# Performance work log

Measured on AMD Instinct MI355X. Metric: run time of the kernel, lower is better.

Reference implementation:

```python
import jax, jax.numpy as jnp
import numpy as np

B, L, D = 1, 2048, 768
H, DH = 12, 64  # n_heads, d_head (D // H)
LN_EPS = 1e-5
DEN_EPS = 1e-6


def setup_inputs() -> dict:
    key = jax.random.key(0)
    ks = jax.random.split(key, 11)
    s = 0.02
    return {
        "x": jax.random.normal(ks[0], (B, L, D), dtype=jnp.float32),
        "W_qkv": jax.random.normal(ks[1], (D, 3 * D), dtype=jnp.float32) * s,
        "b_qkv": jnp.zeros((3 * D,), dtype=jnp.float32),
        "W_sem": jax.random.normal(ks[2], (D, 2 * D), dtype=jnp.float32) * s,
        "b_sem": jnp.zeros((2 * D,), dtype=jnp.float32),
        "W_ctx": jax.random.normal(ks[3], (D, 2 * D), dtype=jnp.float32) * s,
        "b_ctx": jnp.zeros((2 * D,), dtype=jnp.float32),
        "W_proj": jax.random.normal(ks[4], (D, D), dtype=jnp.float32) * s,
        "b_proj": jnp.zeros((D,), dtype=jnp.float32),
        "ln_g": jnp.ones((D,), dtype=jnp.float32),
        "ln_b": jnp.zeros((D,), dtype=jnp.float32),
    }


def _heads(t):
    # [B,L,D] -> [B,H,L,DH]
    return t.reshape(B, L, H, DH).transpose(0, 2, 1, 3)


def reference(x, W_qkv, b_qkv, W_sem, b_sem, W_ctx, b_ctx, W_proj, b_proj, ln_g, ln_b):
    # LayerNorm
    mu = jnp.mean(x, axis=-1, keepdims=True)
    var = jnp.mean(jnp.square(x - mu), axis=-1, keepdims=True)
    x_norm = (x - mu) * jax.lax.rsqrt(var + LN_EPS) * ln_g + ln_b

    qkv = x_norm @ W_qkv + b_qkv
    q, k, v = jnp.split(qkv, 3, axis=-1)

    # interference gate from raw x
    sem = x @ W_sem + b_sem
    sem_amp = jax.nn.softplus(sem[..., :D])
    sem_phase = sem[..., D:]
    ctx = x @ W_ctx + b_ctx
    ctx_amp = jax.nn.softplus(ctx[..., :D])
    ctx_phase = ctx[..., D:]
    gate = jax.nn.sigmoid(sem_amp * ctx_amp * jnp.cos(sem_phase - ctx_phase))
    k = k * gate

    q_f = jax.nn.elu(_heads(q)) + 1.0  # [B,H,L,DH]
    k_f = jax.nn.elu(_heads(k)) + 1.0
    v_f = _heads(v)

    # causal linear attention: cumsum of kv outer products along L
    kv = jnp.einsum("bhld,bhle->bhlde", k_f, v_f)  # [B,H,L,DH,DH]
    kv_cum = jnp.cumsum(kv, axis=2)
    out_num = jnp.einsum("bhld,bhlde->bhle", q_f, kv_cum)  # [B,H,L,DH]

    k_cum = jnp.cumsum(k_f, axis=2)
    out_den = jnp.sum(q_f * k_cum, axis=-1, keepdims=True) + DEN_EPS

    attn = (out_num / out_den).transpose(0, 2, 1, 3).reshape(B, L, D)
    return attn @ W_proj + b_proj
```

## Files before the change

kernel.cpp:

```cpp
#include <hip/hip_runtime.h>
#include <math.h>

#define LSEQ 2048
#define DMODEL 768
#define NHEAD 12
#define DHEAD 64
#define NCHUNK 32
#define NMERGED 5376

typedef unsigned short ushort_t;
typedef __attribute__((ext_vector_type(8))) short short8;
typedef float float4v __attribute__((ext_vector_type(4)));

__device__ __forceinline__ ushort_t f2b(float f) {
    union { float f; unsigned int u; } v; v.f = f;
    unsigned int u = v.u;
    return (ushort_t)((u + 0x7fffu + ((u >> 16) & 1u)) >> 16);
}
__device__ __forceinline__ float b2f(ushort_t u) {
    union { unsigned int u; float f; } v; v.u = ((unsigned int)u) << 16;
    return v.f;
}

__device__ __forceinline__ void gl_lds16(const ushort_t* g, ushort_t* l) {
    __builtin_amdgcn_global_load_lds(
        (const __attribute__((address_space(1))) unsigned int*)g,
        (__attribute__((address_space(3))) unsigned int*)l, 16, 0, 0);
}

__global__ void pre_kernel(const float* __restrict__ x, const float* __restrict__ g,
                           const float* __restrict__ beta, ushort_t* __restrict__ xn,
                           ushort_t* __restrict__ xb,
                           const float* __restrict__ Wq, const float* __restrict__ Ws,
                           const float* __restrict__ Wc, ushort_t* __restrict__ Tm,
                           const float* __restrict__ Wp, ushort_t* __restrict__ Tp) {
    __shared__ float red[4];
    __shared__ float bc;
    __shared__ float tile[32][33];
    int tid = threadIdx.x;
    if (blockIdx.x < 2048) {
        int row = blockIdx.x;
        const float* xr = x + (size_t)row * DMODEL;
        float v0 = xr[tid], v1 = xr[tid + 256], v2 = xr[tid + 512];
        float s = v0 + v1 + v2;
#pragma unroll
        for (int o = 32; o > 0; o >>= 1) s += __shfl_down(s, o);
        if ((tid & 63) == 0) red[tid >> 6] = s;
        __syncthreads();
        if (tid == 0) bc = (red[0] + red[1] + red[2] + red[3]) * (1.0f / DMODEL);
        __syncthreads();
        float mu = bc;
        float d0 = v0 - mu, d1 = v1 - mu, d2 = v2 - mu;
        float vs = d0 * d0 + d1 * d1 + d2 * d2;
        __syncthreads();
#pragma unroll
        for (int o = 32; o > 0; o >>= 1) vs += __shfl_down(vs, o);
        if ((tid & 63) == 0) red[tid >> 6] = vs;
        __syncthreads();
        if (tid == 0) bc = rsqrtf((red[0] + red[1] + red[2] + red[3]) * (1.0f / DMODEL) + 1e-5f);
        __syncthreads();
        float r = bc;
        ushort_t* xo = xn + (size_t)row * DMODEL;
        ushort_t* xc = xb + (size_t)row * DMODEL;
        xo[tid]       = f2b(d0 * r * g[tid]       + beta[tid]);
        xo[tid + 256] = f2b(d1 * r * g[tid + 256] + beta[tid + 256]);
        xo[tid + 512] = f2b(d2 * r * g[tid + 512] + beta[tid + 512]);
        xc[tid]       = f2b(v0);
        xc[tid + 256] = f2b(v1);
        xc[tid + 512] = f2b(v2);
    } else {
        int bid = blockIdx.x - 2048;
        int nb = bid % 72;
        int kb = (bid / 72) % 24;
        int zb = bid / (72 * 24);
        const float* W; ushort_t* Wt; int N;
        switch (zb) {
            case 0: W = Wq; Wt = Tm;                        N = 2304; break;
            case 1: W = Ws; Wt = Tm + (size_t)2304 * 768;   N = 1536; break;
            case 2: W = Wc; Wt = Tm + (size_t)3840 * 768;   N = 1536; break;
            default: W = Wp; Wt = Tp;                       N = 768;  break;
        }
        int nbase = nb * 32;
        if (nbase >= N) return;
        int tr = tid >> 5, tc = tid & 31;
        int kbase = kb * 32;
#pragma unroll
        for (int p = 0; p < 4; p++) {
            int r = p * 8 + tr;
            tile[r][tc] = W[(size_t)(kbase + r) * N + nbase + tc];
        }
        __syncthreads();
#pragma unroll
        for (int p = 0; p < 4; p++) {
            int r = p * 8 + tr;
            Wt[(size_t)(nbase + r) * 768 + kbase + tc] = f2b(tile[tc][r]);
        }
    }
}

__global__ __launch_bounds__(256) void gemm_merged_kernel(
    const ushort_t* __restrict__ Axn, const ushort_t* __restrict__ Axb,
    const ushort_t* __restrict__ Bt,
    const float* __restrict__ b_qkv, const float* __restrict__ b_sem,
    const float* __restrict__ b_ctx, ushort_t* __restrict__ Cb,
    ushort_t* __restrict__ vb) {
    const int K = 768;
    __shared__ ushort_t As[128 * 32];
    __shared__ ushort_t Bs[128 * 32];
    __shared__ ushort_t Ct[128 * 132];
    int tid = threadIdx.x;
    int wave = tid >> 6, lane = tid & 63;
    int wm = (wave >> 1) * 64, wn = (wave & 1) * 64;
    int quad = lane >> 4, l16 = lane & 15;
    int bid = blockIdx.x;
    int xcd = bid & 7, slot = bid >> 3;
    int tile_id = xcd * 84 + slot;
    int m0 = (tile_id & 15) * 128;
    int n0 = (tile_id >> 4) * 128;
    const ushort_t* A = (n0 < 2304) ? Axn : Axb;
    const float* bias = (n0 < 2304) ? (b_qkv + n0) : (n0 < 3840 ? (b_sem + n0 - 2304) : (b_ctx + n0 - 3840));

    int r0 = tid >> 2;
    int kc = ((tid & 3) ^ ((r0 >> 1) & 3)) * 8;
    const ushort_t* Ag0 = A + (size_t)(m0 + r0) * K + kc;
    const ushort_t* Ag1 = A + (size_t)(m0 + 64 + r0) * K + kc;
    const ushort_t* Bg0 = Bt + (size_t)(n0 + r0) * K + kc;
    const ushort_t* Bg1 = Bt + (size_t)(n0 + 64 + r0) * K + kc;
    ushort_t* Al0 = &As[(wave * 64) * 8];
    ushort_t* Al1 = &As[(256 + wave * 64) * 8];
    ushort_t* Bl0 = &Bs[(wave * 64) * 8];
    ushort_t* Bl1 = &Bs[(256 + wave * 64) * 8];

    float4v acc[4][4];
#pragma unroll
    for (int i = 0; i < 4; i++)
#pragma unroll
        for (int j = 0; j < 4; j++)
#pragma unroll
            for (int r = 0; r < 4; r++) acc[i][j][r] = 0.0f;

    for (int k0 = 0; k0 < K; k0 += 32) {
        gl_lds16(Ag0 + k0, Al0);
        gl_lds16(Ag1 + k0, Al1);
        gl_lds16(Bg0 + k0, Bl0);
        gl_lds16(Bg1 + k0, Bl1);
        __syncthreads();
        short8 af[4], bf[4];
#pragma unroll
        for (int i = 0; i < 4; i++) {
            int rr = wm + i * 16 + l16;
            af[i] = *(const short8*)&As[rr * 32 + ((quad ^ ((rr >> 1) & 3)) * 8)];
        }
#pragma unroll
        for (int j = 0; j < 4; j++) {
            int rr = wn + j * 16 + l16;
            bf[j] = *(const short8*)&Bs[rr * 32 + ((quad ^ ((rr >> 1) & 3)) * 8)];
        }
#pragma unroll
        for (int i = 0; i < 4; i++)
#pragma unroll
            for (int j = 0; j < 4; j++)
                acc[i][j] = __builtin_amdgcn_mfma_f32_16x16x32_bf16(af[i], bf[j], acc[i][j], 0, 0, 0);
        __syncthreads();
    }
#pragma unroll
    for (int i = 0; i < 4; i++) {
#pragma unroll
        for (int j = 0; j < 4; j++) {
            int colb = wn + j * 16 + l16;
            float bv = bias[colb];
#pragma unroll
            for (int r = 0; r < 4; r++) {
                int row = wm + i * 16 + quad * 4 + r;
                Ct[row * 132 + colb] = f2b(acc[i][j][r] + bv);
            }
        }
    }
    __syncthreads();
    bool is_v = (n0 >= 1536 && n0 < 2304);
    int rr0 = tid >> 4;
    int cc0 = (tid & 15) * 8;
#pragma unroll
    for (int p = 0; p < 8; p++) {
        int r = p * 16 + rr0;
        uint4 vdat = *(const uint4*)&Ct[r * 132 + cc0];
        int grow = m0 + r;
        if (is_v) {
            *(uint4*)&vb[(size_t)grow * DMODEL + (n0 - 1536) + cc0] = vdat;
        } else {
            *(uint4*)&Cb[(size_t)grow * NMERGED + n0 + cc0] = vdat;
        }
    }
}

__global__ __launch_bounds__(256) void gemm_64_kernel(
    const ushort_t* __restrict__ A, const ushort_t* __restrict__ Bt,
    const float* __restrict__ bias, float* __restrict__ C,
    int N, int K) {
    __shared__ ushort_t As[64 * 32];
    __shared__ ushort_t Bs[64 * 32];
    int tid = threadIdx.x;
    int wave = tid >> 6, lane = tid & 63;
    int wm = (wave >> 1) * 32, wn = (wave & 1) * 32;
    int quad = lane >> 4, l16 = lane & 15;
    int m0 = blockIdx.y * 64, n0 = blockIdx.x * 64;

    int r0 = tid >> 2;
    int kc = ((tid & 3) ^ ((r0 >> 1) & 3)) * 8;
    const ushort_t* Ag = A + (size_t)(m0 + r0) * K + kc;
    const ushort_t* Bg = Bt + (size_t)(n0 + r0) * K + kc;
    ushort_t* Al = &As[(wave * 16) * 32];
    ushort_t* Bl = &Bs[(wave * 16) * 32];

    float4v acc[2][2];
#pragma unroll
    for (int i = 0; i < 2; i++)
#pragma unroll
        for (int j = 0; j < 2; j++)
#pragma unroll
            for (int r = 0; r < 4; r++) acc[i][j][r] = 0.0f;

    for (int k0 = 0; k0 < K; k0 += 32) {
        gl_lds16(Ag + k0, Al);
        gl_lds16(Bg + k0, Bl);
        __syncthreads();
        short8 af[2], bf[2];
#pragma unroll
        for (int i = 0; i < 2; i++) {
            int rr = wm + i * 16 + l16;
            af[i] = *(const short8*)&As[rr * 32 + ((quad ^ ((rr >> 1) & 3)) * 8)];
        }
#pragma unroll
        for (int j = 0; j < 2; j++) {
            int rr = wn + j * 16 + l16;
            bf[j] = *(const short8*)&Bs[rr * 32 + ((quad ^ ((rr >> 1) & 3)) * 8)];
        }
#pragma unroll
        for (int i = 0; i < 2; i++)
#pragma unroll
            for (int j = 0; j < 2; j++)
                acc[i][j] = __builtin_amdgcn_mfma_f32_16x16x32_bf16(af[i], bf[j], acc[i][j], 0, 0, 0);
        __syncthreads();
    }
#pragma unroll
    for (int i = 0; i < 2; i++) {
#pragma unroll
        for (int j = 0; j < 2; j++) {
            int col = n0 + wn + j * 16 + l16;
            float bv = bias[col];
#pragma unroll
            for (int r = 0; r < 4; r++) {
                int row = m0 + wm + i * 16 + quad * 4 + r;
                C[(size_t)row * N + col] = acc[i][j][r] + bv;
            }
        }
    }
}

__device__ __forceinline__ float softplus_f(float x) {
    return (x > 15.f) ? x : log1pf(expf(x));
}

__global__ void gate_feat_kernel(const ushort_t* __restrict__ qscb,
                                 ushort_t* __restrict__ qf, ushort_t* __restrict__ kf) {
    int t = blockIdx.x * 256 + threadIdx.x;
    int l = t / 192, d = (t - l * 192) * 4;
    size_t base = (size_t)l * NMERGED;
    ushort_t sa[4], sp[4], ca[4], cp[4], q[4], k[4];
    *(uint2*)sa = *(const uint2*)&qscb[base + 2304 + d];
    *(uint2*)sp = *(const uint2*)&qscb[base + 3072 + d];
    *(uint2*)ca = *(const uint2*)&qscb[base + 3840 + d];
    *(uint2*)cp = *(const uint2*)&qscb[base + 4608 + d];
    *(uint2*)q  = *(const uint2*)&qscb[base + d];
    *(uint2*)k  = *(const uint2*)&qscb[base + 768 + d];
    ushort_t qo[4], ko[4];
#pragma unroll
    for (int j = 0; j < 4; j++) {
        float amp = softplus_f(b2f(sa[j])) * softplus_f(b2f(ca[j]));
        float tt = amp * cosf(b2f(sp[j]) - b2f(cp[j]));
        float gate = 1.0f / (1.0f + expf(-tt));
        float kv = b2f(k[j]) * gate;
        float qv = b2f(q[j]);
        qo[j] = f2b((qv > 0.f) ? qv + 1.0f : expf(qv));
        ko[j] = f2b((kv > 0.f) ? kv + 1.0f : expf(kv));
    }
    size_t o = (size_t)l * DMODEL + d;
    *(uint2*)&qf[o] = *(uint2*)qo;
    *(uint2*)&kf[o] = *(uint2*)ko;
}

__global__ __launch_bounds__(256) void chunk_sum_mfma(const ushort_t* __restrict__ kf,
                                                      const ushort_t* __restrict__ vb,
                                                      float* __restrict__ S) {
    int h = blockIdx.x % NHEAD;
    int c = blockIdx.x / NHEAD;
    __shared__ ushort_t Kt[64 * 72];
    __shared__ ushort_t Vt[64 * 72];
    int tid = threadIdx.x;
    const size_t hb = (size_t)h * DHEAD;
#pragma unroll
    for (int it = 0; it < 4; it++) {
        int r = it * 16 + (tid >> 4);
        int cc = (tid & 15) * 4;
        int lg = c * 64 + r;
        ushort_t kt4[4], vt4[4];
        *(uint2*)kt4 = *(const uint2*)&kf[(size_t)lg * DMODEL + hb + cc];
        *(uint2*)vt4 = *(const uint2*)&vb[(size_t)lg * DMODEL + hb + cc];
#pragma unroll
        for (int i2 = 0; i2 < 4; i2++) {
            Kt[(cc + i2) * 72 + r] = kt4[i2];
            Vt[(cc + i2) * 72 + r] = vt4[i2];
        }
    }
    __syncthreads();
    int wave = tid >> 6, lane = tid & 63, quad = lane >> 4, l16 = lane & 15;
    int wm = wave * 16;
    float4v acc[4];
#pragma unroll
    for (int jt = 0; jt < 4; jt++)
#pragma unroll
        for (int r = 0; r < 4; r++) acc[jt][r] = 0.0f;
#pragma unroll
    for (int ks = 0; ks < 2; ks++) {
        short8 af = *(const short8*)&Kt[(wm + l16) * 72 + ks * 32 + quad * 8];
#pragma unroll
        for (int jt = 0; jt < 4; jt++) {
            short8 bf = *(const short8*)&Vt[(jt * 16 + l16) * 72 + ks * 32 + quad * 8];
            acc[jt] = __builtin_amdgcn_mfma_f32_16x16x32_bf16(af, bf, acc[jt], 0, 0, 0);
        }
    }
    float* Sp = S + (size_t)(h * NCHUNK + c) * 4160;
#pragma unroll
    for (int jt = 0; jt < 4; jt++) {
        float4 o;
        o.x = acc[jt][0]; o.y = acc[jt][1]; o.z = acc[jt][2]; o.w = acc[jt][3];
        *(float4*)&Sp[(jt * 16 + l16) * 64 + wm + quad * 4] = o;
    }
    if (tid < 64) {
        float s = 0.f;
#pragma unroll
        for (int g = 0; g < 8; g++) {
            short8 kv8 = *(const short8*)&Kt[tid * 72 + g * 8];
#pragma unroll
            for (int i2 = 0; i2 < 8; i2++) s += b2f(((ushort_t*)&kv8)[i2]);
        }
        Sp[4096 + tid] = s;
    }
}

__global__ void prefix_kernel(const float* __restrict__ S, ushort_t* __restrict__ Pb,
                              float* __restrict__ kpf) {
    int h = blockIdx.x;
    int i = blockIdx.y * 256 + threadIdx.x;
    if (i >= 4160) return;
    float v[NCHUNK];
    size_t base = (size_t)h * NCHUNK * 4160 + i;
#pragma unroll
    for (int c2 = 0; c2 < NCHUNK; c2++) v[c2] = S[base + (size_t)c2 * 4160];
    float run = 0.f;
    if (i < 4096) {
        size_t pb = (size_t)h * NCHUNK * 4096 + i;
#pragma unroll
        for (int c2 = 0; c2 < NCHUNK; c2++) {
            Pb[pb + (size_t)c2 * 4096] = f2b(run);
            run += v[c2];
        }
    } else {
        size_t kb = (size_t)h * NCHUNK * 64 + (i - 4096);
#pragma unroll
        for (int c2 = 0; c2 < NCHUNK; c2++) {
            kpf[kb + (size_t)c2 * 64] = run;
            run += v[c2];
        }
    }
}

__global__ __launch_bounds__(256) void attn_out_mfma(const ushort_t* __restrict__ qf,
                                                     const ushort_t* __restrict__ kf,
                                                     const ushort_t* __restrict__ vb,
                                                     const ushort_t* __restrict__ Pb,
                                                     const float* __restrict__ kpf,
                                                     ushort_t* __restrict__ attn) {
    int h = blockIdx.x % NHEAD;
    int c = blockIdx.x / NHEAD;
    __shared__ ushort_t Qs[64 * 72];
    __shared__ ushort_t Ks[64 * 72];
    __shared__ ushort_t Pt[64 * 72];
    __shared__ ushort_t Vt[64 * 72];
    __shared__ float Sc[64 * 68];
    __shared__ float kpl[64];
    __shared__ float denp[4][64];
    __shared__ float dnl[64];
    int tid = threadIdx.x;
    const size_t hb = (size_t)h * DHEAD;
    const size_t pcb = (size_t)(h * NCHUNK + c);
#pragma unroll
    for (int it = 0; it < 2; it++) {
        int chunk = it * 256 + tid;
        int r = chunk >> 3, c8 = (chunk & 7) * 8;
        int lg = c * 64 + r;
        *(uint4*)&Qs[r * 72 + c8] = *(const uint4*)&qf[(size_t)lg * DMODEL + hb + c8];
        *(uint4*)&Ks[r * 72 + c8] = *(const uint4*)&kf[(size_t)lg * DMODEL + hb + c8];
        *(uint4*)&Pt[r * 72 + c8] = *(const uint4*)&Pb[pcb * 4096 + r * 64 + c8];
    }
#pragma unroll
    for (int it = 0; it < 4; it++) {
        int r = it * 16 + (tid >> 4);
        int cc = (tid & 15) * 4;
        int lg = c * 64 + r;
        ushort_t vt4[4];
        *(uint2*)vt4 = *(const uint2*)&vb[(size_t)lg * DMODEL + hb + cc];
#pragma unroll
        for (int i2 = 0; i2 < 4; i2++) Vt[(cc + i2) * 72 + r] = vt4[i2];
    }
    if (tid < 64) kpl[tid] = kpf[pcb * 64 + tid];
    __syncthreads();
    int wave = tid >> 6, lane = tid & 63, quad = lane >> 4, l16 = lane & 15;
    int wm = wave * 16;
    float4v s_acc[4], n_acc[4];
#pragma unroll
    for (int jt = 0; jt < 4; jt++)
#pragma unroll
        for (int r = 0; r < 4; r++) { s_acc[jt][r] = 0.0f; n_acc[jt][r] = 0.0f; }
#pragma unroll
    for (int ks = 0; ks < 2; ks++) {
        short8 aq = *(const short8*)&Qs[(wm + l16) * 72 + ks * 32 + quad * 8];
#pragma unroll
        for (int jt = 0; jt < 4; jt++) {
            short8 bk = *(const short8*)&Ks[(jt * 16 + l16) * 72 + ks * 32 + quad * 8];
            short8 bp = *(const short8*)&Pt[(jt * 16 + l16) * 72 + ks * 32 + quad * 8];
            s_acc[jt] = __builtin_amdgcn_mfma_f32_16x16x32_bf16(aq, bk, s_acc[jt], 0, 0, 0);
            n_acc[jt] = __builtin_amdgcn_mfma_f32_16x16x32_bf16(aq, bp, n_acc[jt], 0, 0, 0);
        }
    }
#pragma unroll
    for (int jt = 0; jt < 4; jt++)
#pragma unroll
        for (int r = 0; r < 4; r++)
            Sc[(wm + quad * 4 + r) * 68 + jt * 16 + l16] = s_acc[jt][r];
    __syncthreads();
    {
        int l = tid & 63, part = tid >> 6;
        float s = 0.f;
#pragma unroll
        for (int jj = 0; jj < 16; jj++) {
            int j = part * 16 + jj;
            float v = Sc[l * 68 + j];
            s += (j <= l) ? v : 0.f;
        }
#pragma unroll
        for (int dd = 0; dd < 16; dd++) {
            int d = part * 16 + dd;
            s += b2f(Qs[l * 72 + d]) * kpl[d];
        }
        denp[part][l] = s;
    }
    __syncthreads();
    if (tid < 64) dnl[tid] = denp[0][tid] + denp[1][tid] + denp[2][tid] + denp[3][tid] + 1e-6f;
    __syncthreads();
#pragma unroll
    for (int ks = 0; ks < 2; ks++) {
        int m = wm + l16;
        float sv[8];
        *(float4*)&sv[0] = *(const float4*)&Sc[m * 68 + ks * 32 + quad * 8];
        *(float4*)&sv[4] = *(const float4*)&Sc[m * 68 + ks * 32 + quad * 8 + 4];
        ushort_t am[8];
#pragma unroll
        for (int i2 = 0; i2 < 8; i2++) {
            int j = ks * 32 + quad * 8 + i2;
            am[i2] = (j <= m) ? f2b(sv[i2]) : (ushort_t)0;
        }
        short8 af = *(short8*)am;
#pragma unroll
        for (int jt = 0; jt < 4; jt++) {
            short8 bv = *(const short8*)&Vt[(jt * 16 + l16) * 72 + ks * 32 + quad * 8];
            n_acc[jt] = __builtin_amdgcn_mfma_f32_16x16x32_bf16(af, bv, n_acc[jt], 0, 0, 0);
        }
    }
#pragma unroll
    for (int jt = 0; jt < 4; jt++) {
        int e = jt * 16 + l16;
#pragma unroll
        for (int r = 0; r < 4; r++) {
            int l = wm + quad * 4 + r;
            float o = n_acc[jt][r] / dnl[l];
            attn[(size_t)(c * 64 + l) * DMODEL + hb + e] = f2b(o);
        }
    }
}

extern "C" void kernel_launch(void* const* d_in, const int* in_sizes, int n_in,
                              void* d_out, int out_size, void* d_ws, size_t ws_size,
                              hipStream_t stream) {
    const float* x      = (const float*)d_in[0];
    const float* W_qkv  = (const float*)d_in[1];
    const float* b_qkv  = (const float*)d_in[2];
    const float* W_sem  = (const float*)d_in[3];
    const float* b_sem  = (const float*)d_in[4];
    const float* W_ctx  = (const float*)d_in[5];
    const float* b_ctx  = (const float*)d_in[6];
    const float* W_proj = (const float*)d_in[7];
    const float* b_proj = (const float*)d_in[8];
    const float* ln_g   = (const float*)d_in[9];
    const float* ln_b   = (const float*)d_in[10];
    float* out = (float*)d_out;
    float* ws  = (float*)d_ws;

    ushort_t* Wt_merged = (ushort_t*)(ws);
    ushort_t* Wt_proj   = (ushort_t*)(ws + 2064384);
    ushort_t* xb        = (ushort_t*)(ws + 2359296);
    ushort_t* xnb       = (ushort_t*)(ws + 3145728);
    ushort_t* qscb      = (ushort_t*)(ws + 3932160);
    ushort_t* qf        = (ushort_t*)(ws + 9437184);
    ushort_t* kf        = (ushort_t*)(ws + 10223616);
    float*    S         = ws + 11010048;
    ushort_t* attnb     = (ushort_t*)(ws + 12607488);
    ushort_t* vb        = (ushort_t*)(ws + 14942208);
    ushort_t* Pb        = (ushort_t*)(ws + 16777216);
    float*    kpf       = ws + 17563648;

    pre_kernel<<<2048 + 72 * 24 * 4, 256, 0, stream>>>(x, ln_g, ln_b, xnb, xb,
                                                       W_qkv, W_sem, W_ctx, Wt_merged,
                                                       W_proj, Wt_proj);

    gemm_merged_kernel<<<672, 256, 0, stream>>>(
        xnb, xb, Wt_merged, b_qkv, b_sem, b_ctx, qscb, vb);

    gate_feat_kernel<<<(LSEQ * DMODEL / 4) / 256, 256, 0, stream>>>(qscb, qf, kf);
    chunk_sum_mfma<<<NHEAD * NCHUNK, 256, 0, stream>>>(kf, vb, S);
    prefix_kernel<<<dim3(NHEAD, 17), 256, 0, stream>>>(S, Pb, kpf);
    attn_out_mfma<<<NHEAD * NCHUNK, 256, 0, stream>>>(qf, kf, vb, Pb, kpf, attnb);

    gemm_64_kernel<<<dim3(768 / 64, LSEQ / 64), 256, 0, stream>>>(attnb, Wt_proj, b_proj, out, 768, 768);
}
```

Before: 157.2 us.

## Fuse gate, chunk-sum, prefix and attention-output into one cooperative kernel

```diff
diff --git a/kernel.cpp b/kernel.cpp
--- a/kernel.cpp
+++ b/kernel.cpp
@@ -1,4 +1,5 @@
 #include <hip/hip_runtime.h>
+#include <hip/hip_cooperative_groups.h>
 #include <math.h>
 
 #define LSEQ 2048
@@ -261,161 +262,136 @@
     return (x > 15.f) ? x : log1pf(expf(x));
 }
 
-__global__ void gate_feat_kernel(const ushort_t* __restrict__ qscb,
-                                 ushort_t* __restrict__ qf, ushort_t* __restrict__ kf) {
-    int t = blockIdx.x * 256 + threadIdx.x;
-    int l = t / 192, d = (t - l * 192) * 4;
-    size_t base = (size_t)l * NMERGED;
-    ushort_t sa[4], sp[4], ca[4], cp[4], q[4], k[4];
-    *(uint2*)sa = *(const uint2*)&qscb[base + 2304 + d];
-    *(uint2*)sp = *(const uint2*)&qscb[base + 3072 + d];
-    *(uint2*)ca = *(const uint2*)&qscb[base + 3840 + d];
-    *(uint2*)cp = *(const uint2*)&qscb[base + 4608 + d];
-    *(uint2*)q  = *(const uint2*)&qscb[base + d];
-    *(uint2*)k  = *(const uint2*)&qscb[base + 768 + d];
-    ushort_t qo[4], ko[4];
-#pragma unroll
-    for (int j = 0; j < 4; j++) {
-        float amp = softplus_f(b2f(sa[j])) * softplus_f(b2f(ca[j]));
-        float tt = amp * cosf(b2f(sp[j]) - b2f(cp[j]));
-        float gate = 1.0f / (1.0f + expf(-tt));
-        float kv = b2f(k[j]) * gate;
-        float qv = b2f(q[j]);
-        qo[j] = f2b((qv > 0.f) ? qv + 1.0f : expf(qv));
-        ko[j] = f2b((kv > 0.f) ? kv + 1.0f : expf(kv));
-    }
-    size_t o = (size_t)l * DMODEL + d;
-    *(uint2*)&qf[o] = *(uint2*)qo;
-    *(uint2*)&kf[o] = *(uint2*)ko;
-}
-
-__global__ __launch_bounds__(256) void chunk_sum_mfma(const ushort_t* __restrict__ kf,
-                                                      const ushort_t* __restrict__ vb,
-                                                      float* __restrict__ S) {
+__global__ __launch_bounds__(256) void attn_fused_kernel(
+    const ushort_t* __restrict__ qscb, const ushort_t* __restrict__ vb,
+    float* __restrict__ S, ushort_t* __restrict__ Pb, float* __restrict__ kpf,
+    ushort_t* __restrict__ attn) {
+    cooperative_groups::grid_group grid = cooperative_groups::this_grid();
     int h = blockIdx.x % NHEAD;
     int c = blockIdx.x / NHEAD;
     __shared__ ushort_t Kt[64 * 72];
+    __shared__ ushort_t Ks[64 * 72];
     __shared__ ushort_t Vt[64 * 72];
-    int tid = threadIdx.x;
-    const size_t hb = (size_t)h * DHEAD;
-#pragma unroll
-    for (int it = 0; it < 4; it++) {
-        int r = it * 16 + (tid >> 4);
-        int cc = (tid & 15) * 4;
-        int lg = c * 64 + r;
-        ushort_t kt4[4], vt4[4];
-        *(uint2*)kt4 = *(const uint2*)&kf[(size_t)lg * DMODEL + hb + cc];
-        *(uint2*)vt4 = *(const uint2*)&vb[(size_t)lg * DMODEL + hb + cc];
-#pragma unroll
-        for (int i2 = 0; i2 < 4; i2++) {
-            Kt[(cc + i2) * 72 + r] = kt4[i2];
-            Vt[(cc + i2) * 72 + r] = vt4[i2];
-        }
-    }
-    __syncthreads();
-    int wave = tid >> 6, lane = tid & 63, quad = lane >> 4, l16 = lane & 15;
-    int wm = wave * 16;
-    float4v acc[4];
-#pragma unroll
-    for (int jt = 0; jt < 4; jt++)
-#pragma unroll
-        for (int r = 0; r < 4; r++) acc[jt][r] = 0.0f;
-#pragma unroll
-    for (int ks = 0; ks < 2; ks++) {
-        short8 af = *(const short8*)&Kt[(wm + l16) * 72 + ks * 32 + quad * 8];
-#pragma unroll
-        for (int jt = 0; jt < 4; jt++) {
-            short8 bf = *(const short8*)&Vt[(jt * 16 + l16) * 72 + ks * 32 + quad * 8];
-            acc[jt] = __builtin_amdgcn_mfma_f32_16x16x32_bf16(af, bf, acc[jt], 0, 0, 0);
-        }
-    }
-    float* Sp = S + (size_t)(h * NCHUNK + c) * 4160;
-#pragma unroll
-    for (int jt = 0; jt < 4; jt++) {
-        float4 o;
-        o.x = acc[jt][0]; o.y = acc[jt][1]; o.z = acc[jt][2]; o.w = acc[jt][3];
-        *(float4*)&Sp[(jt * 16 + l16) * 64 + wm + quad * 4] = o;
-    }
-    if (tid < 64) {
-        float s = 0.f;
-#pragma unroll
-        for (int g = 0; g < 8; g++) {
-            short8 kv8 = *(const short8*)&Kt[tid * 72 + g * 8];
-#pragma unroll
-            for (int i2 = 0; i2 < 8; i2++) s += b2f(((ushort_t*)&kv8)[i2]);
-        }
-        Sp[4096 + tid] = s;
-    }
-}
-
-__global__ void prefix_kernel(const float* __restrict__ S, ushort_t* __restrict__ Pb,
-                              float* __restrict__ kpf) {
-    int h = blockIdx.x;
-    int i = blockIdx.y * 256 + threadIdx.x;
-    if (i >= 4160) return;
-    float v[NCHUNK];
-    size_t base = (size_t)h * NCHUNK * 4160 + i;
-#pragma unroll
-    for (int c2 = 0; c2 < NCHUNK; c2++) v[c2] = S[base + (size_t)c2 * 4160];
-    float run = 0.f;
-    if (i < 4096) {
-        size_t pb = (size_t)h * NCHUNK * 4096 + i;
-#pragma unroll
-        for (int c2 = 0; c2 < NCHUNK; c2++) {
-            Pb[pb + (size_t)c2 * 4096] = f2b(run);
-            run += v[c2];
-        }
-    } else {
-        size_t kb = (size_t)h * NCHUNK * 64 + (i - 4096);
-#pragma unroll
-        for (int c2 = 0; c2 < NCHUNK; c2++) {
-            kpf[kb + (size_t)c2 * 64] = run;
-            run += v[c2];
-        }
-    }
-}
-
-__global__ __launch_bounds__(256) void attn_out_mfma(const ushort_t* __restrict__ qf,
-                                                     const ushort_t* __restrict__ kf,
-                                                     const ushort_t* __restrict__ vb,
-                                                     const ushort_t* __restrict__ Pb,
-                                                     const float* __restrict__ kpf,
-                                                     ushort_t* __restrict__ attn) {
-    int h = blockIdx.x % NHEAD;
-    int c = blockIdx.x / NHEAD;
     __shared__ ushort_t Qs[64 * 72];
-    __shared__ ushort_t Ks[64 * 72];
     __shared__ ushort_t Pt[64 * 72];
-    __shared__ ushort_t Vt[64 * 72];
     __shared__ float Sc[64 * 68];
     __shared__ float kpl[64];
     __shared__ float denp[4][64];
     __shared__ float dnl[64];
     int tid = threadIdx.x;
-    const size_t hb = (size_t)h * DHEAD;
+    const int hb = h * DHEAD;
     const size_t pcb = (size_t)(h * NCHUNK + c);
+    int wave = tid >> 6, lane = tid & 63, quad = lane >> 4, l16 = lane & 15;
+
+#pragma unroll
+    for (int it = 0; it < 4; it++) {
+        int r = it * 16 + (tid >> 4);
+        int cc = (tid & 15) * 4;
+        int lg = c * 64 + r;
+        size_t qb = (size_t)lg * NMERGED + hb + cc;
+        ushort_t k4[4], sa4[4], sp4[4], ca4[4], cp4[4], vt4[4];
+        *(uint2*)k4  = *(const uint2*)&qscb[qb + 768];
+        *(uint2*)sa4 = *(const uint2*)&qscb[qb + 2304];
+        *(uint2*)sp4 = *(const uint2*)&qscb[qb + 3072];
+        *(uint2*)ca4 = *(const uint2*)&qscb[qb + 3840];
+        *(uint2*)cp4 = *(const uint2*)&qscb[qb + 4608];
+        *(uint2*)vt4 = *(const uint2*)&vb[(size_t)lg * DMODEL + hb + cc];
+#pragma unroll
+        for (int i2 = 0; i2 < 4; i2++) {
+            float amp = softplus_f(b2f(sa4[i2])) * softplus_f(b2f(ca4[i2]));
+            float tt = amp * cosf(b2f(sp4[i2]) - b2f(cp4[i2]));
+            float gate = 1.0f / (1.0f + expf(-tt));
+            float kv = b2f(k4[i2]) * gate;
+            ushort_t ko = f2b((kv > 0.f) ? kv + 1.0f : expf(kv));
+            Kt[(cc + i2) * 72 + r] = ko;
+            Ks[r * 72 + cc + i2]   = ko;
+            Vt[(cc + i2) * 72 + r] = vt4[i2];
+        }
+    }
+    __syncthreads();
+    {
+        int wm = wave * 16;
+        float4v acc[4];
+#pragma unroll
+        for (int jt = 0; jt < 4; jt++)
+#pragma unroll
+            for (int r = 0; r < 4; r++) acc[jt][r] = 0.0f;
+#pragma unroll
+        for (int ks = 0; ks < 2; ks++) {
+            short8 af = *(const short8*)&Kt[(wm + l16) * 72 + ks * 32 + quad * 8];
+#pragma unroll
+            for (int jt = 0; jt < 4; jt++) {
+                short8 bf = *(const short8*)&Vt[(jt * 16 + l16) * 72 + ks * 32 + quad * 8];
+                acc[jt] = __builtin_amdgcn_mfma_f32_16x16x32_bf16(af, bf, acc[jt], 0, 0, 0);
+            }
+        }
+        float* Sp = S + pcb * 4160;
+#pragma unroll
+        for (int jt = 0; jt < 4; jt++) {
+            float4 o;
+            o.x = acc[jt][0]; o.y = acc[jt][1]; o.z = acc[jt][2]; o.w = acc[jt][3];
+            *(float4*)&Sp[(jt * 16 + l16) * 64 + wm + quad * 4] = o;
+        }
+        if (tid < 64) {
+            float s = 0.f;
+#pragma unroll
+            for (int g = 0; g < 8; g++) {
+                short8 kv8 = *(const short8*)&Kt[tid * 72 + g * 8];
+#pragma unroll
+                for (int i2 = 0; i2 < 8; i2++) s += b2f(((ushort_t*)&kv8)[i2]);
+            }
+            Sp[4096 + tid] = s;
+        }
+    }
+    __threadfence();
+    grid.sync();
+
+    {
+        int gtid = blockIdx.x * 256 + tid;
+        if (gtid < NHEAD * 4160) {
+            int hh = gtid / 4160, i = gtid - hh * 4160;
+            float v[NCHUNK];
+            size_t base = (size_t)hh * NCHUNK * 4160 + i;
+#pragma unroll
+            for (int c2 = 0; c2 < NCHUNK; c2++) v[c2] = S[base + (size_t)c2 * 4160];
+            float run = 0.f;
+            if (i < 4096) {
+                size_t pb = (size_t)hh * NCHUNK * 4096 + i;
+#pragma unroll
+                for (int c2 = 0; c2 < NCHUNK; c2++) {
+                    Pb[pb + (size_t)c2 * 4096] = f2b(run);
+                    run += v[c2];
+                }
+            } else {
+                size_t kb = (size_t)hh * NCHUNK * 64 + (i - 4096);
+#pragma unroll
+                for (int c2 = 0; c2 < NCHUNK; c2++) {
+                    kpf[kb + (size_t)c2 * 64] = run;
+                    run += v[c2];
+                }
+            }
+        }
+    }
+    __threadfence();
+    grid.sync();
+
 #pragma unroll
     for (int it = 0; it < 2; it++) {
         int chunk = it * 256 + tid;
         int r = chunk >> 3, c8 = (chunk & 7) * 8;
         int lg = c * 64 + r;
-        *(uint4*)&Qs[r * 72 + c8] = *(const uint4*)&qf[(size_t)lg * DMODEL + hb + c8];
-        *(uint4*)&Ks[r * 72 + c8] = *(const uint4*)&kf[(size_t)lg * DMODEL + hb + c8];
+        ushort_t q8[8], qo[8];
+        *(uint4*)q8 = *(const uint4*)&qscb[(size_t)lg * NMERGED + hb + c8];
+#pragma unroll
+        for (int i2 = 0; i2 < 8; i2++) {
+            float qv = b2f(q8[i2]);
+            qo[i2] = f2b((qv > 0.f) ? qv + 1.0f : expf(qv));
+        }
+        *(uint4*)&Qs[r * 72 + c8] = *(uint4*)qo;
         *(uint4*)&Pt[r * 72 + c8] = *(const uint4*)&Pb[pcb * 4096 + r * 64 + c8];
-    }
-#pragma unroll
-    for (int it = 0; it < 4; it++) {
-        int r = it * 16 + (tid >> 4);
-        int cc = (tid & 15) * 4;
-        int lg = c * 64 + r;
-        ushort_t vt4[4];
-        *(uint2*)vt4 = *(const uint2*)&vb[(size_t)lg * DMODEL + hb + cc];
-#pragma unroll
-        for (int i2 = 0; i2 < 4; i2++) Vt[(cc + i2) * 72 + r] = vt4[i2];
     }
     if (tid < 64) kpl[tid] = kpf[pcb * 64 + tid];
     __syncthreads();
-    int wave = tid >> 6, lane = tid & 63, quad = lane >> 4, l16 = lane & 15;
     int wm = wave * 16;
     float4v s_acc[4], n_acc[4];
 #pragma unroll
@@ -511,8 +487,6 @@
     ushort_t* xb        = (ushort_t*)(ws + 2359296);
     ushort_t* xnb       = (ushort_t*)(ws + 3145728);
     ushort_t* qscb      = (ushort_t*)(ws + 3932160);
-    ushort_t* qf        = (ushort_t*)(ws + 9437184);
-    ushort_t* kf        = (ushort_t*)(ws + 10223616);
     float*    S         = ws + 11010048;
     ushort_t* attnb     = (ushort_t*)(ws + 12607488);
     ushort_t* vb        = (ushort_t*)(ws + 14942208);
@@ -526,10 +500,9 @@
     gemm_merged_kernel<<<672, 256, 0, stream>>>(
         xnb, xb, Wt_merged, b_qkv, b_sem, b_ctx, qscb, vb);
 
-    gate_feat_kernel<<<(LSEQ * DMODEL / 4) / 256, 256, 0, stream>>>(qscb, qf, kf);
-    chunk_sum_mfma<<<NHEAD * NCHUNK, 256, 0, stream>>>(kf, vb, S);
-    prefix_kernel<<<dim3(NHEAD, 17), 256, 0, stream>>>(S, Pb, kpf);
-    attn_out_mfma<<<NHEAD * NCHUNK, 256, 0, stream>>>(qf, kf, vb, Pb, kpf, attnb);
+    void* cargs[] = {(void*)&qscb, (void*)&vb, (void*)&S, (void*)&Pb, (void*)&kpf, (void*)&attnb};
+    hipLaunchCooperativeKernel((void*)attn_fused_kernel, dim3(NHEAD * NCHUNK), dim3(256),
+                               cargs, 0, stream);
 
     gemm_64_kernel<<<dim3(768 / 64, LSEQ / 64), 256, 0, stream>>>(attnb, Wt_proj, b_proj, out, 768, 768);
 }
```

Result: slower. 335.4 us (+113.3%).

## Fuse chunk prefix scan into attention output kernel with XCD-aware tile mapping

Applied to the files above, without the earlier changes.

```diff
diff --git a/kernel.cpp b/kernel.cpp
--- a/kernel.cpp
+++ b/kernel.cpp
@@ -348,41 +348,16 @@
     }
 }
 
-__global__ void prefix_kernel(const float* __restrict__ S, ushort_t* __restrict__ Pb,
-                              float* __restrict__ kpf) {
-    int h = blockIdx.x;
-    int i = blockIdx.y * 256 + threadIdx.x;
-    if (i >= 4160) return;
-    float v[NCHUNK];
-    size_t base = (size_t)h * NCHUNK * 4160 + i;
-#pragma unroll
-    for (int c2 = 0; c2 < NCHUNK; c2++) v[c2] = S[base + (size_t)c2 * 4160];
-    float run = 0.f;
-    if (i < 4096) {
-        size_t pb = (size_t)h * NCHUNK * 4096 + i;
-#pragma unroll
-        for (int c2 = 0; c2 < NCHUNK; c2++) {
-            Pb[pb + (size_t)c2 * 4096] = f2b(run);
-            run += v[c2];
-        }
-    } else {
-        size_t kb = (size_t)h * NCHUNK * 64 + (i - 4096);
-#pragma unroll
-        for (int c2 = 0; c2 < NCHUNK; c2++) {
-            kpf[kb + (size_t)c2 * 64] = run;
-            run += v[c2];
-        }
-    }
-}
-
 __global__ __launch_bounds__(256) void attn_out_mfma(const ushort_t* __restrict__ qf,
                                                      const ushort_t* __restrict__ kf,
                                                      const ushort_t* __restrict__ vb,
-                                                     const ushort_t* __restrict__ Pb,
-                                                     const float* __restrict__ kpf,
+                                                     const float* __restrict__ S,
                                                      ushort_t* __restrict__ attn) {
-    int h = blockIdx.x % NHEAD;
-    int c = blockIdx.x / NHEAD;
+    int bid = blockIdx.x;
+    int xcd = bid & 7, slot = bid >> 3;
+    int tile = xcd * 48 + slot;
+    int h = tile >> 5;
+    int c = tile & 31;
     __shared__ ushort_t Qs[64 * 72];
     __shared__ ushort_t Ks[64 * 72];
     __shared__ ushort_t Pt[64 * 72];
@@ -393,7 +368,6 @@
     __shared__ float dnl[64];
     int tid = threadIdx.x;
     const size_t hb = (size_t)h * DHEAD;
-    const size_t pcb = (size_t)(h * NCHUNK + c);
 #pragma unroll
     for (int it = 0; it < 2; it++) {
         int chunk = it * 256 + tid;
@@ -401,7 +375,6 @@
         int lg = c * 64 + r;
         *(uint4*)&Qs[r * 72 + c8] = *(const uint4*)&qf[(size_t)lg * DMODEL + hb + c8];
         *(uint4*)&Ks[r * 72 + c8] = *(const uint4*)&kf[(size_t)lg * DMODEL + hb + c8];
-        *(uint4*)&Pt[r * 72 + c8] = *(const uint4*)&Pb[pcb * 4096 + r * 64 + c8];
     }
 #pragma unroll
     for (int it = 0; it < 4; it++) {
@@ -413,7 +386,32 @@
 #pragma unroll
         for (int i2 = 0; i2 < 4; i2++) Vt[(cc + i2) * 72 + r] = vt4[i2];
     }
-    if (tid < 64) kpl[tid] = kpf[pcb * 64 + tid];
+    {
+        float4 pacc[4];
+#pragma unroll
+        for (int j = 0; j < 4; j++) { pacc[j].x = 0.f; pacc[j].y = 0.f; pacc[j].z = 0.f; pacc[j].w = 0.f; }
+        float kpacc = 0.f;
+        const float* Sh = S + (size_t)h * NCHUNK * 4160;
+        for (int c2 = 0; c2 < c; c2++) {
+            const float* Sp = Sh + (size_t)c2 * 4160;
+#pragma unroll
+            for (int j = 0; j < 4; j++) {
+                float4 v4 = *(const float4*)&Sp[j * 1024 + tid * 4];
+                pacc[j].x += v4.x; pacc[j].y += v4.y; pacc[j].z += v4.z; pacc[j].w += v4.w;
+            }
+            if (tid < 64) kpacc += Sp[4096 + tid];
+        }
+#pragma unroll
+        for (int j = 0; j < 4; j++) {
+            int i = j * 1024 + tid * 4;
+            int e = i >> 6, d = i & 63;
+            ushort_t o4[4];
+            o4[0] = f2b(pacc[j].x); o4[1] = f2b(pacc[j].y);
+            o4[2] = f2b(pacc[j].z); o4[3] = f2b(pacc[j].w);
+            *(uint2*)&Pt[e * 72 + d] = *(uint2*)o4;
+        }
+        if (tid < 64) kpl[tid] = kpacc;
+    }
     __syncthreads();
     int wave = tid >> 6, lane = tid & 63, quad = lane >> 4, l16 = lane & 15;
     int wm = wave * 16;
@@ -516,8 +514,6 @@
     float*    S         = ws + 11010048;
     ushort_t* attnb     = (ushort_t*)(ws + 12607488);
     ushort_t* vb        = (ushort_t*)(ws + 14942208);
-    ushort_t* Pb        = (ushort_t*)(ws + 16777216);
-    float*    kpf       = ws + 17563648;
 
     pre_kernel<<<2048 + 72 * 24 * 4, 256, 0, stream>>>(x, ln_g, ln_b, xnb, xb,
                                                        W_qkv, W_sem, W_ctx, Wt_merged,
@@ -528,8 +524,7 @@
 
     gate_feat_kernel<<<(LSEQ * DMODEL / 4) / 256, 256, 0, stream>>>(qscb, qf, kf);
     chunk_sum_mfma<<<NHEAD * NCHUNK, 256, 0, stream>>>(kf, vb, S);
-    prefix_kernel<<<dim3(NHEAD, 17), 256, 0, stream>>>(S, Pb, kpf);
-    attn_out_mfma<<<NHEAD * NCHUNK, 256, 0, stream>>>(qf, kf, vb, Pb, kpf, attnb);
+    attn_out_mfma<<<NHEAD * NCHUNK, 256, 0, stream>>>(qf, kf, vb, S, attnb);
 
     gemm_64_kernel<<<dim3(768 / 64, LSEQ / 64), 256, 0, stream>>>(attnb, Wt_proj, b_proj, out, 768, 768);
 }
```

After: 165.4 us. 1.05x slower.
